# Kernel tuning notes

Hardware: AMD Instinct MI355X
Metric: run time of the kernel (lower is better)

The kernel has to match this reference:

```python
import jax, jax.numpy as jnp
import numpy as np

B, S, D = 8, 2048, 256
EXP = 4
NEG = -1e9
EPS = 1e-5


def layer_norm(x, w, b):
    mu = jnp.mean(x, axis=-1, keepdims=True)
    var = jnp.var(x, axis=-1, keepdims=True)
    return (x - mu) * jax.lax.rsqrt(var + EPS) * w + b


def setup_inputs() -> dict:
    key = jax.random.key(0)
    ks = jax.random.split(key, 8)
    x = jax.random.normal(ks[0], (B, S, D), dtype=jnp.float32)
    r_mat = jax.random.normal(ks[1], (B, S, S), dtype=jnp.float32)
    attn_mask = jax.random.randint(ks[2], (S, S), 0, 2).astype(jnp.float32)
    pad_mask = jax.random.randint(ks[3], (B, 1, S), 0, 2).astype(jnp.float32)
    w1 = jax.random.normal(ks[4], (D, EXP * D), dtype=jnp.float32) / np.sqrt(D)
    b1 = jnp.zeros((EXP * D,), dtype=jnp.float32)
    w2 = jax.random.normal(ks[5], (EXP * D, D), dtype=jnp.float32) / np.sqrt(EXP * D)
    b2 = jnp.zeros((D,), dtype=jnp.float32)
    ln1_w = jnp.ones((D,), dtype=jnp.float32)
    ln1_b = jnp.zeros((D,), dtype=jnp.float32)
    ln2_w = jnp.ones((D,), dtype=jnp.float32)
    ln2_b = jnp.zeros((D,), dtype=jnp.float32)
    return {"x": x, "r_mat": r_mat, "attn_mask": attn_mask, "pad_mask": pad_mask,
            "ln1_w": ln1_w, "ln1_b": ln1_b, "ln2_w": ln2_w, "ln2_b": ln2_b,
            "w1": w1, "b1": b1, "w2": w2, "b2": b2}


def reference(x, r_mat, attn_mask, pad_mask, ln1_w, ln1_b, ln2_w, ln2_b, w1, b1, w2, b2):
    # sublayer 0: pre-LN + InrAwaSA + residual
    h = layer_norm(x, ln1_w, ln1_b)                       # [B,S,D]
    scale = jnp.sqrt(jnp.float32(D))
    scores = jnp.einsum("bqd,bkd->bqk", h, h) / scale      # [B,S,S]
    # mask r_mat by pad_mask [B,1,S] and attn_mask [1,S,S], then softmax
    rm = jnp.where(pad_mask == 0.0, NEG, r_mat)
    rm = jnp.where(attn_mask[None] == 0.0, NEG, rm)
    scores = scores + jax.nn.softmax(rm, axis=-1)
    # NOTE: the torch source calls scores.masked_fill(...) non-in-place and
    # discards the result, so scores are NOT re-masked here (faithful no-op).
    prob = jax.nn.softmax(scores, axis=-1)
    x = x + jnp.einsum("bqk,bkd->bqd", prob, h)
    # sublayer 1: pre-LN + FFN + residual (dropout is identity in eval)
    h2 = layer_norm(x, ln2_w, ln2_b)
    ffn = jax.nn.relu(h2 @ w1 + b1) @ w2 + b2
    return x + ffn
```

## Files before the change

kernel.cpp:

```cpp
#include <hip/hip_runtime.h>
#include <stdint.h>

#define NB 8
#define SS 2048
#define DD 256
#define NEGV -1e9f

typedef __attribute__((ext_vector_type(8))) __bf16 bf16x8;
typedef __attribute__((ext_vector_type(4))) float f32x4;

union U16 { uint4 u; bf16x8 b; unsigned short us[8]; };

__device__ __forceinline__ unsigned short tobf(float v) {
  union { float f; uint32_t u; } c; c.f = v;
  uint32_t r = (c.u + 0x7fffu + ((c.u >> 16) & 1u)) >> 16;
  return (unsigned short)r;
}
__device__ __forceinline__ float frombf(unsigned short v) {
  union { uint32_t u; float f; } c; c.u = ((uint32_t)v) << 16;
  return c.f;
}

__device__ __forceinline__ void glds16(const unsigned short* g, unsigned short* l) {
  __builtin_amdgcn_global_load_lds(
      (const __attribute__((address_space(1))) uint32_t*)g,
      (__attribute__((address_space(3))) uint32_t*)l, 16, 0, 0);
}

__device__ __forceinline__ void stage_tile(const unsigned short* src, int ld,
                                           unsigned short* lbuf, int w, int lane) {
  int rl = lane >> 2;
  int cs = (lane & 3) * 8;
  glds16(src + (size_t)(w * 32 + rl) * ld + cs, lbuf + w * 1024);
  glds16(src + (size_t)(w * 32 + 16 + rl) * ld + cs, lbuf + w * 1024 + 512);
}

template <int NSTEPS>
__device__ __forceinline__ void gemm128_tile(
    const unsigned short* __restrict__ A, int lda,
    const unsigned short* __restrict__ Bt, int ldb,
    unsigned short* lA, unsigned short* lB, f32x4 (&acc)[4][4]) {
  const int w = threadIdx.x >> 6, lane = threadIdx.x & 63;
  const int lr = lane & 15, lg = lane >> 4;
  const int wm = w >> 1, wn = w & 1;
#pragma unroll
  for (int i = 0; i < 4; ++i)
#pragma unroll
    for (int j = 0; j < 4; ++j) acc[i][j] = (f32x4){0.f, 0.f, 0.f, 0.f};
  stage_tile(A, lda, lA, w, lane);
  stage_tile(Bt, ldb, lB, w, lane);
  __syncthreads();
  for (int s = 0; s < NSTEPS; ++s) {
    const unsigned short* cA = lA + (s & 1) * 4096;
    const unsigned short* cB = lB + (s & 1) * 4096;
    if (s + 1 < NSTEPS) {
      stage_tile(A + (s + 1) * 32, lda, lA + ((s + 1) & 1) * 4096, w, lane);
      stage_tile(Bt + (s + 1) * 32, ldb, lB + ((s + 1) & 1) * 4096, w, lane);
    }
    bf16x8 am[4], bn[4];
#pragma unroll
    for (int i = 0; i < 4; ++i) {
      U16 u; u.u = *(const uint4*)(cA + (wm * 64 + i * 16 + lr) * 32 + lg * 8);
      am[i] = u.b;
      U16 v; v.u = *(const uint4*)(cB + (wn * 64 + i * 16 + lr) * 32 + lg * 8);
      bn[i] = v.b;
    }
#pragma unroll
    for (int i = 0; i < 4; ++i)
#pragma unroll
      for (int j = 0; j < 4; ++j)
        acc[i][j] = __builtin_amdgcn_mfma_f32_16x16x32_bf16(am[i], bn[j], acc[i][j], 0, 0, 0);
    __syncthreads();
  }
}

__global__ void ln_kernel(const float* __restrict__ in, const float* __restrict__ w,
                          const float* __restrict__ bparm, unsigned short* __restrict__ outb) {
  int row = blockIdx.x * 4 + (threadIdx.x >> 6);
  int lane = threadIdx.x & 63;
  const float* xr = in + (size_t)row * DD;
  float4 v = *(const float4*)(xr + lane * 4);
  float s = v.x + v.y + v.z + v.w;
  float s2 = v.x * v.x + v.y * v.y + v.z * v.z + v.w * v.w;
#pragma unroll
  for (int m = 1; m < 64; m <<= 1) { s += __shfl_xor(s, m); s2 += __shfl_xor(s2, m); }
  float mu = s * (1.f / DD);
  float var = s2 * (1.f / DD) - mu * mu;
  float rs = rsqrtf(var + 1e-5f);
  float4 wv = *(const float4*)(w + lane * 4);
  float4 bv = *(const float4*)(bparm + lane * 4);
  ushort4 o;
  o.x = tobf((v.x - mu) * rs * wv.x + bv.x);
  o.y = tobf((v.y - mu) * rs * wv.y + bv.y);
  o.z = tobf((v.z - mu) * rs * wv.z + bv.z);
  o.w = tobf((v.w - mu) * rs * wv.w + bv.w);
  *(ushort4*)(outb + (size_t)row * DD + lane * 4) = o;
}

__global__ void transpose_kernel(const unsigned short* __restrict__ in,
                                 unsigned short* __restrict__ out) {
  __shared__ unsigned short tile[64][72];
  int bid = blockIdx.x;
  int b = bid >> 7;
  int rest = bid & 127;
  int st = rest >> 2, dt = rest & 3;
  int s0 = st * 64, d0 = dt * 64;
  int t = threadIdx.x;
  int r = t >> 2, cs = (t & 3) * 16;
  const unsigned short* src = in + ((size_t)b * SS + s0 + r) * DD + d0 + cs;
  *(uint4*)&tile[r][cs] = *(const uint4*)src;
  *(uint4*)&tile[r][cs + 8] = *(const uint4*)(src + 8);
  __syncthreads();
  union { unsigned short us[16]; uint4 u[2]; } tmp;
  int dr = t >> 2, sseg = (t & 3) * 16;
#pragma unroll
  for (int j = 0; j < 16; ++j) tmp.us[j] = tile[sseg + j][dr];
  unsigned short* dst = out + ((size_t)b * DD + d0 + dr) * SS + s0 + sseg;
  *(uint4*)dst = tmp.u[0];
  *(uint4*)(dst + 8) = tmp.u[1];
}

__global__ __launch_bounds__(256) void qk_kernel(
    const unsigned short* __restrict__ hb,
    unsigned short* __restrict__ S) {
  __shared__ unsigned short lA[2 * 4096], lB[2 * 4096];
  int bid = blockIdx.x;
  int b = bid & 7;
  int tile = bid >> 3;
  int mb = tile >> 4, nb = tile & 15;
  const unsigned short* A = hb + (size_t)(b * SS + mb * 128) * DD;
  const unsigned short* Bt = hb + (size_t)(b * SS + nb * 128) * DD;
  f32x4 acc[4][4];
  gemm128_tile<8>(A, DD, Bt, DD, lA, lB, acc);
  int w = threadIdx.x >> 6, lane = threadIdx.x & 63;
  int lr = lane & 15, lg = lane >> 4;
  int wm = w >> 1, wn = w & 1;
  unsigned short* Sb = S + (size_t)b * SS * SS;
#pragma unroll
  for (int i = 0; i < 4; ++i)
#pragma unroll
    for (int j = 0; j < 4; ++j)
#pragma unroll
      for (int r = 0; r < 4; ++r) {
        int m = mb * 128 + wm * 64 + i * 16 + lg * 4 + r;
        int n = nb * 128 + wn * 64 + j * 16 + lr;
        Sb[(size_t)m * SS + n] = tobf(acc[i][j][r] * 0.0625f);
      }
}

__global__ __launch_bounds__(256) void smfuse_kernel(
    const float* __restrict__ r_mat,
    const float* __restrict__ attn,
    const float* __restrict__ pad,
    unsigned short* __restrict__ S) {
  int row = blockIdx.x * 4 + (threadIdx.x >> 6);
  int lane = threadIdx.x & 63;
  int b = row >> 11, q = row & 2047;
  const float* rrow = r_mat + (size_t)row * SS;
  const float* arow = attn + (size_t)q * SS;
  const float* prow = pad + (size_t)b * SS;
  unsigned short* srow = S + (size_t)row * SS;

  float rm[32];
  float mx = -__builtin_inff();
#pragma unroll
  for (int i = 0; i < 8; ++i) {
    int c = i * 256 + lane * 4;
    float4 rv = *(const float4*)(rrow + c);
    float4 av = *(const float4*)(arow + c);
    float4 pv = *(const float4*)(prow + c);
    float v0 = (pv.x == 0.f || av.x == 0.f) ? NEGV : rv.x;
    float v1 = (pv.y == 0.f || av.y == 0.f) ? NEGV : rv.y;
    float v2 = (pv.z == 0.f || av.z == 0.f) ? NEGV : rv.z;
    float v3 = (pv.w == 0.f || av.w == 0.f) ? NEGV : rv.w;
    rm[i * 4 + 0] = v0; rm[i * 4 + 1] = v1; rm[i * 4 + 2] = v2; rm[i * 4 + 3] = v3;
    mx = fmaxf(mx, fmaxf(fmaxf(v0, v1), fmaxf(v2, v3)));
  }
#pragma unroll
  for (int m = 1; m < 64; m <<= 1) mx = fmaxf(mx, __shfl_xor(mx, m));
  float sum = 0.f;
#pragma unroll
  for (int j = 0; j < 32; ++j) { rm[j] = __expf(rm[j] - mx); sum += rm[j]; }
#pragma unroll
  for (int m = 1; m < 64; m <<= 1) sum += __shfl_xor(sum, m);
  float inv = 1.f / sum;

  float sc[32];
  float mx2 = -__builtin_inff();
#pragma unroll
  for (int i = 0; i < 8; ++i) {
    int c = i * 256 + lane * 4;
    ushort4 sv = *(const ushort4*)(srow + c);
    float s0 = frombf(sv.x) + rm[i * 4 + 0] * inv;
    float s1 = frombf(sv.y) + rm[i * 4 + 1] * inv;
    float s2 = frombf(sv.z) + rm[i * 4 + 2] * inv;
    float s3 = frombf(sv.w) + rm[i * 4 + 3] * inv;
    sc[i * 4 + 0] = s0; sc[i * 4 + 1] = s1; sc[i * 4 + 2] = s2; sc[i * 4 + 3] = s3;
    mx2 = fmaxf(mx2, fmaxf(fmaxf(s0, s1), fmaxf(s2, s3)));
  }
#pragma unroll
  for (int m = 1; m < 64; m <<= 1) mx2 = fmaxf(mx2, __shfl_xor(mx2, m));
  float sum2 = 0.f;
#pragma unroll
  for (int j = 0; j < 32; ++j) { sc[j] = __expf(sc[j] - mx2); sum2 += sc[j]; }
#pragma unroll
  for (int m = 1; m < 64; m <<= 1) sum2 += __shfl_xor(sum2, m);
  float inv2 = 1.f / sum2;
#pragma unroll
  for (int i = 0; i < 8; ++i) {
    int c = i * 256 + lane * 4;
    ushort4 o;
    o.x = tobf(sc[i * 4 + 0] * inv2);
    o.y = tobf(sc[i * 4 + 1] * inv2);
    o.z = tobf(sc[i * 4 + 2] * inv2);
    o.w = tobf(sc[i * 4 + 3] * inv2);
    *(ushort4*)(srow + c) = o;
  }
}

__global__ __launch_bounds__(256) void pv_kernel(
    const unsigned short* __restrict__ P,
    const unsigned short* __restrict__ hbT,
    unsigned short* __restrict__ pvp) {
  __shared__ unsigned short lA[2 * 4096], lB[2 * 4096];
  int bid = blockIdx.x;
  int b = bid & 7;
  int rest = bid >> 3;
  int ks = rest & 3;
  int rest2 = rest >> 2;
  int nb = rest2 & 1, mb = rest2 >> 1;
  const unsigned short* A = P + (size_t)(b * SS + mb * 128) * SS + ks * 512;
  const unsigned short* Bt = hbT + (size_t)(b * DD + nb * 128) * SS + ks * 512;
  f32x4 acc[4][4];
  gemm128_tile<16>(A, SS, Bt, SS, lA, lB, acc);
  int w = threadIdx.x >> 6, lane = threadIdx.x & 63;
  int lr = lane & 15, lg = lane >> 4;
  int wm = w >> 1, wn = w & 1;
  unsigned short* O = pvp + ((size_t)(ks << 14) + (b << 11)) * DD;
#pragma unroll
  for (int i = 0; i < 4; ++i)
#pragma unroll
    for (int j = 0; j < 4; ++j)
#pragma unroll
      for (int r = 0; r < 4; ++r) {
        int m = mb * 128 + wm * 64 + i * 16 + lg * 4 + r;
        int n = nb * 128 + wn * 64 + j * 16 + lr;
        O[(size_t)m * DD + n] = tobf(acc[i][j][r]);
      }
}

__global__ __launch_bounds__(256) void pvreduce_kernel(
    const unsigned short* __restrict__ pvp,
    const float* __restrict__ x,
    const float* __restrict__ ln2w,
    const float* __restrict__ ln2b,
    float* __restrict__ out,
    unsigned short* __restrict__ h2b) {
  int r = blockIdx.x * 4 + (threadIdx.x >> 6);
  int lane = threadIdx.x & 63;
  int c = lane * 4;
  float o[4] = {0.f, 0.f, 0.f, 0.f};
#pragma unroll
  for (int ks = 0; ks < 4; ++ks) {
    ushort4 pk = *(const ushort4*)(pvp + ((size_t)(ks << 14) + r) * DD + c);
    o[0] += frombf(pk.x); o[1] += frombf(pk.y);
    o[2] += frombf(pk.z); o[3] += frombf(pk.w);
  }
  float4 xv = *(const float4*)(x + (size_t)r * DD + c);
  float val[4] = {o[0] + xv.x, o[1] + xv.y, o[2] + xv.z, o[3] + xv.w};
  float4 ov = {val[0], val[1], val[2], val[3]};
  *(float4*)(out + (size_t)r * DD + c) = ov;
  float s = val[0] + val[1] + val[2] + val[3];
  float s2 = val[0] * val[0] + val[1] * val[1] + val[2] * val[2] + val[3] * val[3];
#pragma unroll
  for (int m = 1; m < 64; m <<= 1) { s += __shfl_xor(s, m); s2 += __shfl_xor(s2, m); }
  float mu = s * (1.f / DD);
  float var = s2 * (1.f / DD) - mu * mu;
  float rsv = rsqrtf(var + 1e-5f);
  float4 wv = *(const float4*)(ln2w + c);
  float4 bv = *(const float4*)(ln2b + c);
  ushort4 h;
  h.x = tobf((val[0] - mu) * rsv * wv.x + bv.x);
  h.y = tobf((val[1] - mu) * rsv * wv.y + bv.y);
  h.z = tobf((val[2] - mu) * rsv * wv.z + bv.z);
  h.w = tobf((val[3] - mu) * rsv * wv.w + bv.w);
  *(ushort4*)(h2b + (size_t)r * DD + c) = h;
}

__global__ void wconv_kernel(const float* __restrict__ src, unsigned short* __restrict__ dst,
                             int K, int N) {
  int k = blockIdx.x;
  for (int n = threadIdx.x; n < N; n += 256)
    dst[(size_t)n * K + k] = tobf(src[(size_t)k * N + n]);
}

__global__ __launch_bounds__(256) void ffn1_kernel(
    const unsigned short* __restrict__ A0,
    const unsigned short* __restrict__ Bt0,
    const float* __restrict__ bias,
    unsigned short* __restrict__ Out) {
  __shared__ unsigned short lA[2 * 4096], lB[2 * 4096];
  int bid = blockIdx.x;
  int nb = bid & 7, mb = bid >> 3;
  const unsigned short* A = A0 + (size_t)(mb * 128) * 256;
  const unsigned short* Bt = Bt0 + (size_t)(nb * 128) * 256;
  f32x4 acc[4][4];
  gemm128_tile<8>(A, 256, Bt, 256, lA, lB, acc);
  int w = threadIdx.x >> 6, lane = threadIdx.x & 63;
  int lr = lane & 15, lg = lane >> 4;
  int wm = w >> 1, wn = w & 1;
#pragma unroll
  for (int i = 0; i < 4; ++i)
#pragma unroll
    for (int j = 0; j < 4; ++j)
#pragma unroll
      for (int r = 0; r < 4; ++r) {
        int m = mb * 128 + wm * 64 + i * 16 + lg * 4 + r;
        int n = nb * 128 + wn * 64 + j * 16 + lr;
        float v = fmaxf(acc[i][j][r] + bias[n], 0.f);
        Out[(size_t)m * 1024 + n] = tobf(v);
      }
}

__global__ __launch_bounds__(256) void ffn2_kernel(
    const unsigned short* __restrict__ A0,
    const unsigned short* __restrict__ Bt0,
    unsigned short* __restrict__ f2p) {
  __shared__ unsigned short lA[2 * 4096], lB[2 * 4096];
  int bid = blockIdx.x;
  int ks = bid & 3;
  int rest = bid >> 2;
  int nb = rest & 1, mb = rest >> 1;
  const unsigned short* A = A0 + (size_t)(mb * 128) * 1024 + ks * 256;
  const unsigned short* Bt = Bt0 + (size_t)(nb * 128) * 1024 + ks * 256;
  f32x4 acc[4][4];
  gemm128_tile<8>(A, 1024, Bt, 1024, lA, lB, acc);
  int w = threadIdx.x >> 6, lane = threadIdx.x & 63;
  int lr = lane & 15, lg = lane >> 4;
  int wm = w >> 1, wn = w & 1;
  unsigned short* O = f2p + (size_t)(ks << 14) * DD;
#pragma unroll
  for (int i = 0; i < 4; ++i)
#pragma unroll
    for (int j = 0; j < 4; ++j)
#pragma unroll
      for (int r = 0; r < 4; ++r) {
        int m = mb * 128 + wm * 64 + i * 16 + lg * 4 + r;
        int n = nb * 128 + wn * 64 + j * 16 + lr;
        O[(size_t)m * DD + n] = tobf(acc[i][j][r]);
      }
}

__global__ __launch_bounds__(256) void f2reduce_kernel(
    const unsigned short* __restrict__ f2p,
    const float* __restrict__ bias,
    float* __restrict__ out) {
  int r = blockIdx.x * 4 + (threadIdx.x >> 6);
  int lane = threadIdx.x & 63;
  int c = lane * 4;
  float o[4] = {0.f, 0.f, 0.f, 0.f};
#pragma unroll
  for (int ks = 0; ks < 4; ++ks) {
    ushort4 pk = *(const ushort4*)(f2p + ((size_t)(ks << 14) + r) * DD + c);
    o[0] += frombf(pk.x); o[1] += frombf(pk.y);
    o[2] += frombf(pk.z); o[3] += frombf(pk.w);
  }
  float4 bv = *(const float4*)(bias + c);
  float* orow = out + (size_t)r * DD + c;
  float4 cur = *(const float4*)orow;
  float4 res = {cur.x + o[0] + bv.x, cur.y + o[1] + bv.y,
                cur.z + o[2] + bv.z, cur.w + o[3] + bv.w};
  *(float4*)orow = res;
}

extern "C" void kernel_launch(void* const* d_in, const int* in_sizes, int n_in,
                              void* d_out, int out_size, void* d_ws, size_t ws_size,
                              hipStream_t stream) {
  const float* x     = (const float*)d_in[0];
  const float* r_mat = (const float*)d_in[1];
  const float* attn  = (const float*)d_in[2];
  const float* pad   = (const float*)d_in[3];
  const float* ln1w  = (const float*)d_in[4];
  const float* ln1b  = (const float*)d_in[5];
  const float* ln2w  = (const float*)d_in[6];
  const float* ln2b  = (const float*)d_in[7];
  const float* w1    = (const float*)d_in[8];
  const float* b1    = (const float*)d_in[9];
  const float* w2    = (const float*)d_in[10];
  const float* b2    = (const float*)d_in[11];
  float* out = (float*)d_out;

  uint8_t* ws = (uint8_t*)d_ws;
  unsigned short* hb   = (unsigned short*)(ws + 0);
  unsigned short* hbT  = (unsigned short*)(ws + 8388608);
  unsigned short* h2b  = (unsigned short*)(ws + 16777216);
  unsigned short* w1bT = (unsigned short*)(ws + 25165824);
  unsigned short* w2bT = (unsigned short*)(ws + 25690112);
  unsigned short* S    = (unsigned short*)(ws + 33554432);
  unsigned short* pvp  = (unsigned short*)(ws + 100663296);
  unsigned short* t    = S;
  unsigned short* f2p  = pvp;

  hipLaunchKernelGGL(ln_kernel, dim3(4096), dim3(256), 0, stream, x, ln1w, ln1b, hb);
  hipLaunchKernelGGL(transpose_kernel, dim3(1024), dim3(256), 0, stream, hb, hbT);
  hipLaunchKernelGGL(qk_kernel, dim3(2048), dim3(256), 0, stream, hb, S);
  hipLaunchKernelGGL(smfuse_kernel, dim3(4096), dim3(256), 0, stream, r_mat, attn, pad, S);
  hipLaunchKernelGGL(pv_kernel, dim3(1024), dim3(256), 0, stream, S, hbT, pvp);
  hipLaunchKernelGGL(pvreduce_kernel, dim3(4096), dim3(256), 0, stream,
                     pvp, x, ln2w, ln2b, out, h2b);
  hipLaunchKernelGGL(wconv_kernel, dim3(256), dim3(256), 0, stream, w1, w1bT, 256, 1024);
  hipLaunchKernelGGL(wconv_kernel, dim3(1024), dim3(256), 0, stream, w2, w2bT, 1024, 256);
  hipLaunchKernelGGL(ffn1_kernel, dim3(1024), dim3(256), 0, stream, h2b, w1bT, b1, t);
  hipLaunchKernelGGL(ffn2_kernel, dim3(1024), dim3(256), 0, stream, t, w2bT, f2p);
  hipLaunchKernelGGL(f2reduce_kernel, dim3(4096), dim3(256), 0, stream, f2p, b2, out);
}
```

Before: 201.5 us.

## Stage GEMM epilogues through LDS, exploit QK symmetry, tile weight conversion

GEMM epilogues now write the accumulator tile to shared memory (padded stride) and then emit coalesced 16-byte row stores, replacing scattered 2-byte global writes. The QK kernel exploits the symmetry of h·hᵀ: only upper-triangular tiles compute, and each writes both its tile and its transpose, roughly halving QK MFMA work. The two weight-conversion launches are merged into one LDS-tiled transpose kernel with coalesced reads and writes. Costs include an extra LDS round trip and barrier per tile, plus idle early-exit blocks in QK.

```diff
diff --git a/kernel.cpp b/kernel.cpp
--- a/kernel.cpp
+++ b/kernel.cpp
@@ -5,6 +5,7 @@
 #define SS 2048
 #define DD 256
 #define NEGV -1e9f
+#define LDSW 136
 
 typedef __attribute__((ext_vector_type(8))) __bf16 bf16x8;
 typedef __attribute__((ext_vector_type(4))) float f32x4;
@@ -39,7 +40,9 @@
 __device__ __forceinline__ void gemm128_tile(
     const unsigned short* __restrict__ A, int lda,
     const unsigned short* __restrict__ Bt, int ldb,
-    unsigned short* lA, unsigned short* lB, f32x4 (&acc)[4][4]) {
+    unsigned short* smem, f32x4 (&acc)[4][4]) {
+  unsigned short* lA = smem;
+  unsigned short* lB = smem + 8192;
   const int w = threadIdx.x >> 6, lane = threadIdx.x & 63;
   const int lr = lane & 15, lg = lane >> 4;
   const int wm = w >> 1, wn = w & 1;
@@ -74,6 +77,40 @@
   }
 }
 
+template <int MODE, int TRANS>
+__device__ __forceinline__ void epi128(
+    unsigned short* smem, f32x4 (&acc)[4][4],
+    unsigned short* dst, int ldd, float scale, const float* bias, int n0) {
+  const int tid = threadIdx.x;
+  const int w = tid >> 6, lane = tid & 63;
+  const int lr = lane & 15, lg = lane >> 4;
+  const int wm = w >> 1, wn = w & 1;
+#pragma unroll
+  for (int i = 0; i < 4; ++i)
+#pragma unroll
+    for (int j = 0; j < 4; ++j) {
+      int col = wn * 64 + j * 16 + lr;
+#pragma unroll
+      for (int r = 0; r < 4; ++r) {
+        int row = wm * 64 + i * 16 + lg * 4 + r;
+        float v = acc[i][j][r];
+        if (MODE == 0) v = v * scale;
+        if (MODE == 2) v = fmaxf(v + bias[n0 + col], 0.f);
+        if (TRANS) smem[col * LDSW + row] = tobf(v);
+        else       smem[row * LDSW + col] = tobf(v);
+      }
+    }
+  __syncthreads();
+  int row = tid >> 1, half = (tid & 1) * 64;
+  const unsigned short* s = smem + row * LDSW + half;
+  unsigned short* d = dst + (size_t)row * ldd + half;
+  uint4 vv[8];
+#pragma unroll
+  for (int k = 0; k < 8; ++k) vv[k] = *(const uint4*)(s + k * 8);
+#pragma unroll
+  for (int k = 0; k < 8; ++k) *(uint4*)(d + k * 8) = vv[k];
+}
+
 __global__ void ln_kernel(const float* __restrict__ in, const float* __restrict__ w,
                           const float* __restrict__ bparm, unsigned short* __restrict__ outb) {
   int row = blockIdx.x * 4 + (threadIdx.x >> 6);
@@ -123,29 +160,24 @@
 __global__ __launch_bounds__(256) void qk_kernel(
     const unsigned short* __restrict__ hb,
     unsigned short* __restrict__ S) {
-  __shared__ unsigned short lA[2 * 4096], lB[2 * 4096];
+  __shared__ unsigned short smem[128 * LDSW];
   int bid = blockIdx.x;
   int b = bid & 7;
-  int tile = bid >> 3;
-  int mb = tile >> 4, nb = tile & 15;
+  int t = bid >> 3;
+  int mb = t >> 4, nb = t & 15;
+  if (mb > nb) return;
   const unsigned short* A = hb + (size_t)(b * SS + mb * 128) * DD;
   const unsigned short* Bt = hb + (size_t)(b * SS + nb * 128) * DD;
   f32x4 acc[4][4];
-  gemm128_tile<8>(A, DD, Bt, DD, lA, lB, acc);
-  int w = threadIdx.x >> 6, lane = threadIdx.x & 63;
-  int lr = lane & 15, lg = lane >> 4;
-  int wm = w >> 1, wn = w & 1;
+  gemm128_tile<8>(A, DD, Bt, DD, smem, acc);
   unsigned short* Sb = S + (size_t)b * SS * SS;
-#pragma unroll
-  for (int i = 0; i < 4; ++i)
-#pragma unroll
-    for (int j = 0; j < 4; ++j)
-#pragma unroll
-      for (int r = 0; r < 4; ++r) {
-        int m = mb * 128 + wm * 64 + i * 16 + lg * 4 + r;
-        int n = nb * 128 + wn * 64 + j * 16 + lr;
-        Sb[(size_t)m * SS + n] = tobf(acc[i][j][r] * 0.0625f);
-      }
+  epi128<0, 0>(smem, acc, Sb + (size_t)(mb * 128) * SS + nb * 128, SS,
+               0.0625f, nullptr, 0);
+  if (mb != nb) {
+    __syncthreads();
+    epi128<0, 1>(smem, acc, Sb + (size_t)(nb * 128) * SS + mb * 128, SS,
+                 0.0625f, nullptr, 0);
+  }
 }
 
 __global__ __launch_bounds__(256) void smfuse_kernel(
@@ -222,7 +254,7 @@
     const unsigned short* __restrict__ P,
     const unsigned short* __restrict__ hbT,
     unsigned short* __restrict__ pvp) {
-  __shared__ unsigned short lA[2 * 4096], lB[2 * 4096];
+  __shared__ unsigned short smem[128 * LDSW];
   int bid = blockIdx.x;
   int b = bid & 7;
   int rest = bid >> 3;
@@ -232,21 +264,9 @@
   const unsigned short* A = P + (size_t)(b * SS + mb * 128) * SS + ks * 512;
   const unsigned short* Bt = hbT + (size_t)(b * DD + nb * 128) * SS + ks * 512;
   f32x4 acc[4][4];
-  gemm128_tile<16>(A, SS, Bt, SS, lA, lB, acc);
-  int w = threadIdx.x >> 6, lane = threadIdx.x & 63;
-  int lr = lane & 15, lg = lane >> 4;
-  int wm = w >> 1, wn = w & 1;
-  unsigned short* O = pvp + ((size_t)(ks << 14) + (b << 11)) * DD;
-#pragma unroll
-  for (int i = 0; i < 4; ++i)
-#pragma unroll
-    for (int j = 0; j < 4; ++j)
-#pragma unroll
-      for (int r = 0; r < 4; ++r) {
-        int m = mb * 128 + wm * 64 + i * 16 + lg * 4 + r;
-        int n = nb * 128 + wn * 64 + j * 16 + lr;
-        O[(size_t)m * DD + n] = tobf(acc[i][j][r]);
-      }
+  gemm128_tile<16>(A, SS, Bt, SS, smem, acc);
+  unsigned short* dst = pvp + ((size_t)(ks << 14) + (b << 11) + mb * 128) * DD + nb * 128;
+  epi128<1, 0>(smem, acc, dst, DD, 1.f, nullptr, 0);
 }
 
 __global__ __launch_bounds__(256) void pvreduce_kernel(
@@ -287,11 +307,29 @@
   *(ushort4*)(h2b + (size_t)r * DD + c) = h;
 }
 
-__global__ void wconv_kernel(const float* __restrict__ src, unsigned short* __restrict__ dst,
-                             int K, int N) {
-  int k = blockIdx.x;
-  for (int n = threadIdx.x; n < N; n += 256)
-    dst[(size_t)n * K + k] = tobf(src[(size_t)k * N + n]);
+__global__ void wconv_kernel(const float* __restrict__ w1, unsigned short* __restrict__ w1bT,
+                             const float* __restrict__ w2, unsigned short* __restrict__ w2bT) {
+  __shared__ unsigned short tile[64][72];
+  int bid = blockIdx.x;
+  const float* src; unsigned short* dst; int K, N, t;
+  if (bid < 64) { src = w1; dst = w1bT; K = 256; N = 1024; t = bid; }
+  else          { src = w2; dst = w2bT; K = 1024; N = 256; t = bid - 64; }
+  int nt = N >> 6;
+  int kt = t / nt, ntb = t % nt;
+  int k0 = kt * 64, n0 = ntb * 64;
+  int tt = threadIdx.x;
+  int r = tt >> 2, c4 = (tt & 3) * 16;
+  const float* s = src + (size_t)(k0 + r) * N + n0 + c4;
+#pragma unroll
+  for (int j = 0; j < 16; ++j) tile[r][c4 + j] = tobf(s[j]);
+  __syncthreads();
+  union { unsigned short us[16]; uint4 u[2]; } tmp;
+  int nr = tt >> 2, ks = (tt & 3) * 16;
+#pragma unroll
+  for (int j = 0; j < 16; ++j) tmp.us[j] = tile[ks + j][nr];
+  unsigned short* d = dst + (size_t)(n0 + nr) * K + k0 + ks;
+  *(uint4*)d = tmp.u[0];
+  *(uint4*)(d + 8) = tmp.u[1];
 }
 
 __global__ __launch_bounds__(256) void ffn1_kernel(
@@ -299,34 +337,22 @@
     const unsigned short* __restrict__ Bt0,
     const float* __restrict__ bias,
     unsigned short* __restrict__ Out) {
-  __shared__ unsigned short lA[2 * 4096], lB[2 * 4096];
+  __shared__ unsigned short smem[128 * LDSW];
   int bid = blockIdx.x;
   int nb = bid & 7, mb = bid >> 3;
   const unsigned short* A = A0 + (size_t)(mb * 128) * 256;
   const unsigned short* Bt = Bt0 + (size_t)(nb * 128) * 256;
   f32x4 acc[4][4];
-  gemm128_tile<8>(A, 256, Bt, 256, lA, lB, acc);
-  int w = threadIdx.x >> 6, lane = threadIdx.x & 63;
-  int lr = lane & 15, lg = lane >> 4;
-  int wm = w >> 1, wn = w & 1;
-#pragma unroll
-  for (int i = 0; i < 4; ++i)
-#pragma unroll
-    for (int j = 0; j < 4; ++j)
-#pragma unroll
-      for (int r = 0; r < 4; ++r) {
-        int m = mb * 128 + wm * 64 + i * 16 + lg * 4 + r;
-        int n = nb * 128 + wn * 64 + j * 16 + lr;
-        float v = fmaxf(acc[i][j][r] + bias[n], 0.f);
-        Out[(size_t)m * 1024 + n] = tobf(v);
-      }
+  gemm128_tile<8>(A, 256, Bt, 256, smem, acc);
+  epi128<2, 0>(smem, acc, Out + (size_t)(mb * 128) * 1024 + nb * 128, 1024,
+               1.f, bias, nb * 128);
 }
 
 __global__ __launch_bounds__(256) void ffn2_kernel(
     const unsigned short* __restrict__ A0,
     const unsigned short* __restrict__ Bt0,
     unsigned short* __restrict__ f2p) {
-  __shared__ unsigned short lA[2 * 4096], lB[2 * 4096];
+  __shared__ unsigned short smem[128 * LDSW];
   int bid = blockIdx.x;
   int ks = bid & 3;
   int rest = bid >> 2;
@@ -334,21 +360,9 @@
   const unsigned short* A = A0 + (size_t)(mb * 128) * 1024 + ks * 256;
   const unsigned short* Bt = Bt0 + (size_t)(nb * 128) * 1024 + ks * 256;
   f32x4 acc[4][4];
-  gemm128_tile<8>(A, 1024, Bt, 1024, lA, lB, acc);
-  int w = threadIdx.x >> 6, lane = threadIdx.x & 63;
-  int lr = lane & 15, lg = lane >> 4;
-  int wm = w >> 1, wn = w & 1;
-  unsigned short* O = f2p + (size_t)(ks << 14) * DD;
-#pragma unroll
-  for (int i = 0; i < 4; ++i)
-#pragma unroll
-    for (int j = 0; j < 4; ++j)
-#pragma unroll
-      for (int r = 0; r < 4; ++r) {
-        int m = mb * 128 + wm * 64 + i * 16 + lg * 4 + r;
-        int n = nb * 128 + wn * 64 + j * 16 + lr;
-        O[(size_t)m * DD + n] = tobf(acc[i][j][r]);
-      }
+  gemm128_tile<8>(A, 1024, Bt, 1024, smem, acc);
+  unsigned short* dst = f2p + ((size_t)(ks << 14) + mb * 128) * DD + nb * 128;
+  epi128<1, 0>(smem, acc, dst, DD, 1.f, nullptr, 0);
 }
 
 __global__ __launch_bounds__(256) void f2reduce_kernel(
@@ -408,8 +422,7 @@
   hipLaunchKernelGGL(pv_kernel, dim3(1024), dim3(256), 0, stream, S, hbT, pvp);
   hipLaunchKernelGGL(pvreduce_kernel, dim3(4096), dim3(256), 0, stream,
                      pvp, x, ln2w, ln2b, out, h2b);
-  hipLaunchKernelGGL(wconv_kernel, dim3(256), dim3(256), 0, stream, w1, w1bT, 256, 1024);
-  hipLaunchKernelGGL(wconv_kernel, dim3(1024), dim3(256), 0, stream, w2, w2bT, 1024, 256);
+  hipLaunchKernelGGL(wconv_kernel, dim3(128), dim3(256), 0, stream, w1, w1bT, w2, w2bT);
   hipLaunchKernelGGL(ffn1_kernel, dim3(1024), dim3(256), 0, stream, h2b, w1bT, b1, t);
   hipLaunchKernelGGL(ffn2_kernel, dim3(1024), dim3(256), 0, stream, t, w2bT, f2p);
   hipLaunchKernelGGL(f2reduce_kernel, dim3(4096), dim3(256), 0, stream, f2p, b2, out);
```

After: 217.1 us. +7.8%, slower.
